# Kernel optimization log

Measured on AMD Instinct MI355X. Metric: run time of the kernel, lower is better.

The kernel has to match this reference:

```python
import jax, jax.numpy as jnp
import numpy as np

N_CHANNELS = 512
D_K = 64
N_HEADS = N_CHANNELS // D_K  # 8
SCALE = 1.0 / np.sqrt(np.sqrt(D_K))
EPS = 1e-8


def pixnorm(x, axis=-1):
    return x * jax.lax.rsqrt(jnp.mean(x * x, axis=axis, keepdims=True) + EPS)


def setup_inputs() -> dict:
    key = jax.random.key(0)
    k1, k2, k3 = jax.random.split(key, 3)
    x = jax.random.normal(k1, (16, N_CHANNELS, 32, 32), dtype=jnp.float32)
    # 1x1 conv weights (bias=False) stored as [out, in]
    w_proj = jax.random.normal(k2, (3 * N_CHANNELS, N_CHANNELS), dtype=jnp.float32) * (1.0 / np.sqrt(N_CHANNELS))
    w_out = jax.random.normal(k3, (N_CHANNELS, N_CHANNELS), dtype=jnp.float32) * (1.0 / np.sqrt(N_CHANNELS))
    return {"x": x, "w_proj": w_proj, "w_out": w_out}


def reference(x, w_proj, w_out):
    B, C, H, W = x.shape
    S = H * W
    # tokens: [B, S, C]
    xt = x.reshape(B, C, S).transpose(0, 2, 1)
    # 1x1 conv projection -> [B, S, 3C]
    h = jnp.einsum('bsc,oc->bso', xt, w_proj)
    qkv = h.reshape(B, S, N_HEADS, 3 * D_K)
    q, k, v = jnp.split(qkv, 3, axis=-1)  # each [B, S, H, d]
    q = pixnorm(q)
    k = pixnorm(k)
    v = pixnorm(v)
    attn = jnp.einsum('bihd,bjhd->bijh', q * SCALE, k * SCALE)
    attn = jax.nn.softmax(attn, axis=2)
    res = jnp.einsum('bijh,bjhd->bihd', attn, v)  # [B, S, H, d]
    res = res.reshape(B, S, C)
    res = jnp.einsum('bsc,oc->bso', res, w_out)
    res = res.transpose(0, 2, 1).reshape(B, C, H, W)
    return x + res
```

## Files before the change

kernel.cpp:

```cpp
#include <hip/hip_runtime.h>
#include <hip/hip_bf16.h>
#include <math.h>

typedef float f32x4 __attribute__((ext_vector_type(4)));
typedef __bf16 bf16x8 __attribute__((ext_vector_type(8)));
typedef __bf16 bf16x4 __attribute__((ext_vector_type(4)));
typedef unsigned u32x4 __attribute__((ext_vector_type(4)));

#define DEVFN static __device__ __forceinline__

DEVFN void gload16(const void* g, void* l) {
  __builtin_amdgcn_global_load_lds(
      (const __attribute__((address_space(1))) unsigned int*)g,
      (__attribute__((address_space(3))) unsigned int*)l, 16, 0, 0);
}

DEVFN f32x4 mfma16(bf16x8 a, bf16x8 b, f32x4 c) {
  return __builtin_amdgcn_mfma_f32_16x16x32_bf16(a, b, c, 0, 0, 0);
}

DEVFN unsigned cvtpk(float lo, float hi) {
  unsigned r;
  asm("v_cvt_pk_bf16_f32 %0, %1, %2" : "=v"(r) : "v"(lo), "v"(hi));
  return r;
}

#define WAITV4() asm volatile("s_waitcnt vmcnt(4)" ::: "memory")
#define WAITV0() asm volatile("s_waitcnt vmcnt(0)" ::: "memory")

__global__ __launch_bounds__(256) void transpose_x_k(
    const float* __restrict__ x, __bf16* __restrict__ xt,
    const float* __restrict__ wp, const float* __restrict__ wo,
    __bf16* __restrict__ wpb, __bf16* __restrict__ wob) {
  __shared__ float tile[64][65];
  int b = blockIdx.z, c0 = blockIdx.y * 64, s0 = blockIdx.x * 64;
  int t = threadIdx.x;
  int r = t >> 2, q = (t & 3) << 4;
  const float* src = x + ((size_t)(b * 512 + c0 + r)) * 1024 + s0 + q;
#pragma unroll
  for (int i = 0; i < 4; i++) {
    float4 f = *reinterpret_cast<const float4*>(src + i * 4);
    tile[r][q + i * 4 + 0] = f.x;
    tile[r][q + i * 4 + 1] = f.y;
    tile[r][q + i * 4 + 2] = f.z;
    tile[r][q + i * 4 + 3] = f.w;
  }
  int lid = (blockIdx.z * 8 + blockIdx.y) * 16 + blockIdx.x;
  int wi = lid * 512 + t * 2;
  if (wi < 786432) {
    float2 f = *reinterpret_cast<const float2*>(wp + wi);
    wpb[wi] = (__bf16)f.x;
    wpb[wi + 1] = (__bf16)f.y;
  } else {
    int j = wi - 786432;
    float2 f = *reinterpret_cast<const float2*>(wo + j);
    wob[j] = (__bf16)f.x;
    wob[j + 1] = (__bf16)f.y;
  }
  __syncthreads();
  bf16x8 o0, o1;
#pragma unroll
  for (int i = 0; i < 8; i++) o0[i] = (__bf16)tile[q + i][r];
#pragma unroll
  for (int i = 0; i < 8; i++) o1[i] = (__bf16)tile[q + 8 + i][r];
  __bf16* dst = xt + ((size_t)(b * 1024 + s0 + r)) * 512 + c0 + q;
  *reinterpret_cast<bf16x8*>(dst) = o0;
  *reinterpret_cast<bf16x8*>(dst + 8) = o1;
}

template <int MODE>
__global__ __launch_bounds__(256, 4) void gemm_bt_k(
    const __bf16* __restrict__ A, const __bf16* __restrict__ Bt,
    float* __restrict__ Cf, const float* __restrict__ Xres,
    __bf16* __restrict__ Qo, __bf16* __restrict__ Ko, __bf16* __restrict__ Vto) {
  __shared__ __attribute__((aligned(16))) char smem[49152];
  int p = blockIdx.x, xcd = p & 7, idx = p >> 3;
  int m0, n0, z;
  if (MODE == 2) {
    m0 = (xcd * 16 + idx / 12) * 128;
    n0 = (idx % 12) * 128;
    z = 0;
  } else {
    z = xcd * 2 + idx / 32;
    int rem = idx % 32;
    m0 = (rem >> 3) * 128;
    n0 = (rem & 7) * 128;
    Bt += (size_t)z * (1024L * 512);
  }
  int tid = threadIdx.x, wave = tid >> 6, lane = tid & 63;
  int fr = lane & 15, fq = lane >> 4;
  int wm = (wave >> 1) * 64, wn = (wave & 1) * 64;
  f32x4 acc[4][4] = {};
  int offs[2], rr[2], scc[2];
#pragma unroll
  for (int i = 0; i < 2; i++) {
    offs[i] = wave * 2048 + i * 1024 + lane * 16;
    rr[i] = offs[i] >> 6;
    scc[i] = (offs[i] & 63) ^ (((rr[i] ^ (rr[i] >> 2)) & 3) << 4);
  }
  int rdsw = (fr ^ (fr >> 2)) & 3;
  const char* Ap = (const char*)A;
  const char* Bp = (const char*)Bt;

#define GSTAGE(k0_, slot_)                                                      \
  {                                                                             \
    char* as_ = smem + (slot_)*16384;                                           \
    char* bs_ = as_ + 8192;                                                     \
    _Pragma("unroll") for (int i = 0; i < 2; i++)                               \
        gload16(Ap + (size_t)(m0 + rr[i]) * 1024 + (k0_)*2 + scc[i],            \
                as_ + offs[i]);                                                 \
    _Pragma("unroll") for (int i = 0; i < 2; i++)                               \
        gload16(Bp + (size_t)(n0 + rr[i]) * 1024 + (k0_)*2 + scc[i],            \
                bs_ + offs[i]);                                                 \
  }

  GSTAGE(0, 0);
  GSTAGE(32, 1);
#pragma unroll
  for (int t = 0; t < 16; t++) {
    if (t < 15) WAITV4(); else WAITV0();
    __builtin_amdgcn_s_barrier();
    __builtin_amdgcn_sched_barrier(0);
    const char* as = smem + (t % 3) * 16384;
    const char* bs = as + 8192;
    bf16x8 af[4], bfr[4];
#pragma unroll
    for (int mi = 0; mi < 4; mi++)
      af[mi] = *reinterpret_cast<const bf16x8*>(
          as + (wm + mi * 16 + fr) * 64 + ((fq ^ rdsw) << 4));
#pragma unroll
    for (int ni = 0; ni < 4; ni++)
      bfr[ni] = *reinterpret_cast<const bf16x8*>(
          bs + (wn + ni * 16 + fr) * 64 + ((fq ^ rdsw) << 4));
    if (t + 2 < 16) GSTAGE((t + 2) * 32, (t + 2) % 3);
    __builtin_amdgcn_s_setprio(1);
#pragma unroll
    for (int mi = 0; mi < 4; mi++)
#pragma unroll
      for (int ni = 0; ni < 4; ni++)
        acc[mi][ni] = mfma16(af[mi], bfr[ni], acc[mi][ni]);
    __builtin_amdgcn_s_setprio(0);
  }
#undef GSTAGE

  if (MODE == 1) {
    float* Co = Cf + (size_t)z * (512L * 1024);
    const float* Xr = Xres + (size_t)z * (512L * 1024);
#pragma unroll
    for (int mi = 0; mi < 4; mi++)
#pragma unroll
      for (int i = 0; i < 4; i++) {
        int row = m0 + wm + mi * 16 + fq * 4 + i;
#pragma unroll
        for (int ni = 0; ni < 4; ni++) {
          size_t idxo = (size_t)row * 1024 + n0 + wn + ni * 16 + fr;
          Co[idxo] = acc[mi][ni][i] + Xr[idxo];
        }
      }
  } else {
    int g0 = n0 + wn;
    int head = g0 / 192;
    int grp = (g0 >> 6) % 3;
    int b = m0 >> 10, sb = m0 & 1023;
    int bh = b * 8 + head;
    float nrm[4][4];
#pragma unroll
    for (int mi = 0; mi < 4; mi++)
#pragma unroll
      for (int i = 0; i < 4; i++) {
        float ss = 0.f;
#pragma unroll
        for (int ni = 0; ni < 4; ni++) ss += acc[mi][ni][i] * acc[mi][ni][i];
#pragma unroll
        for (int off = 1; off < 16; off <<= 1) ss += __shfl_xor(ss, off);
        float nv = rsqrtf(ss * (1.0f / 64.0f) + 1e-8f);
        if (grp == 0) nv *= 0.18033688011112042f;
        nrm[mi][i] = nv;
      }
    if (grp < 2) {
      __bf16* dst = (grp == 0 ? Qo : Ko) + (size_t)bh * 65536;
#pragma unroll
      for (int mi = 0; mi < 4; mi++)
#pragma unroll
        for (int i = 0; i < 4; i++) {
          int s = sb + wm + mi * 16 + fq * 4 + i;
#pragma unroll
          for (int ni = 0; ni < 4; ni++)
            dst[(size_t)s * 64 + ni * 16 + fr] = (__bf16)(acc[mi][ni][i] * nrm[mi][i]);
        }
    }
    __syncthreads();
    if (grp == 2) {
#pragma unroll
      for (int mi = 0; mi < 4; mi++)
#pragma unroll
        for (int i = 0; i < 4; i++) {
          int r = wm + mi * 16 + fq * 4 + i;
#pragma unroll
          for (int ni = 0; ni < 4; ni++) {
            int col2 = (2 * (ni * 16 + fr)) ^ ((r & 31) << 2);
            *(__bf16*)(smem + r * 128 + col2) = (__bf16)(acc[mi][ni][i] * nrm[mi][i]);
          }
        }
    }
    __syncthreads();
    if (grp == 2) {
      int sl = wm + lane;
      int l = sl & 63;
      int pl = ((l >> 2) & 3) * 16 + (l >> 4) * 4 + (l & 3);
      __bf16* vdst = Vto + (size_t)bh * 65536 + sb + (sl & 64) + pl;
#pragma unroll 8
      for (int d = 0; d < 64; d++) {
        __bf16 v = *(const __bf16*)(smem + sl * 128 + ((2 * d) ^ ((sl & 31) << 2)));
        vdst[(size_t)d * 1024] = v;
      }
    }
  }
}

__global__ __launch_bounds__(256, 4) void attn_k(const __bf16* __restrict__ Q,
                                                 const __bf16* __restrict__ Kb,
                                                 const __bf16* __restrict__ Vt,
                                                 __bf16* __restrict__ Res) {
  __shared__ __attribute__((aligned(16))) char lds[32768];
  int p = blockIdx.x;
  int v = (p & 7) * 128 + (p >> 3);
  int qt = v & 7, bh = v >> 3;
  int wave = threadIdx.x >> 6, lane = threadIdx.x & 63;
  int fr = lane & 15, fq = lane >> 4;
  const __bf16* Qb = Q + (size_t)bh * 65536;
  const char* Kbase = (const char*)(Kb + (size_t)bh * 65536);
  const char* Vbase = (const char*)(Vt + (size_t)bh * 65536);
  bf16x8 qf[2][2];
#pragma unroll
  for (int qs = 0; qs < 2; qs++)
#pragma unroll
    for (int kk = 0; kk < 2; kk++)
      qf[qs][kk] = *reinterpret_cast<const bf16x8*>(
          Qb + (size_t)(qt * 128 + qs * 64 + wave * 16 + fr) * 64 + kk * 32 + fq * 8);

  bf16x8 ones;
#pragma unroll
  for (int j = 0; j < 8; j++) ones[j] = (__bf16)1.0f;

  f32x4 oa[2][4] = {};
  f32x4 lacc[2] = {};

  int o0 = wave * 2048 + lane * 16;
  int o1 = o0 + 1024;
  int r0 = o0 >> 7, c0 = o0 & 127, r1 = o1 >> 7, c1 = o1 & 127;
  int s0 = c0 ^ ((r0 & 7) << 4), s1 = c1 ^ ((r1 & 7) << 4);
  int swr = (fr & 7) << 4;

#define STAGE(kt_, buf_)                                                        \
  {                                                                             \
    char* ks_ = lds + (buf_)*8192;                                              \
    char* vs_ = lds + 16384 + (buf_)*8192;                                      \
    gload16(Kbase + (size_t)(kt_)*8192 + r0 * 128 + s0, ks_ + o0);              \
    gload16(Kbase + (size_t)(kt_)*8192 + r1 * 128 + s1, ks_ + o1);              \
    gload16(Vbase + (size_t)r0 * 2048 + (kt_)*128 + s0, vs_ + o0);              \
    gload16(Vbase + (size_t)r1 * 2048 + (kt_)*128 + s1, vs_ + o1);              \
  }

#define QKT(buf_)                                                               \
  {                                                                             \
    const char* ksc_ = lds + (buf_)*8192;                                       \
    __builtin_amdgcn_s_setprio(1);                                              \
    _Pragma("unroll") for (int ni = 0; ni < 4; ni++) {                          \
      bf16x8 kf0 = *reinterpret_cast<const bf16x8*>(                            \
          ksc_ + (ni * 16 + fr) * 128 + ((fq * 16) ^ swr));                     \
      bf16x8 kf1 = *reinterpret_cast<const bf16x8*>(                            \
          ksc_ + (ni * 16 + fr) * 128 + ((64 + fq * 16) ^ swr));                \
      _Pragma("unroll") for (int qs = 0; qs < 2; qs++) {                        \
        sa[qs][ni] = mfma16(kf0, qf[qs][0], sa[qs][ni]);                        \
        sa[qs][ni] = mfma16(kf1, qf[qs][1], sa[qs][ni]);                        \
      }                                                                         \
    }                                                                           \
    __builtin_amdgcn_s_setprio(0);                                              \
  }

  STAGE(0, 0);
  STAGE(1, 1);
  WAITV4();
  __builtin_amdgcn_s_barrier();
  __builtin_amdgcn_sched_barrier(0);
  f32x4 sa[2][4] = {};
  QKT(0);
  for (int kt = 0; kt < 16; kt++) {
    int cur = kt & 1;
    const char* vsc = lds + 16384 + cur * 8192;
    bf16x8 pb[2][2];
#pragma unroll
    for (int qs = 0; qs < 2; qs++) {
#pragma unroll
      for (int ni = 0; ni < 4; ni++)
#pragma unroll
        for (int i = 0; i < 4; i++)
          sa[qs][ni][i] = __builtin_amdgcn_exp2f(sa[qs][ni][i]);
#pragma unroll
      for (int kk2 = 0; kk2 < 2; kk2++) {
        u32x4 u;
        u[0] = cvtpk(sa[qs][2 * kk2][0], sa[qs][2 * kk2][1]);
        u[1] = cvtpk(sa[qs][2 * kk2][2], sa[qs][2 * kk2][3]);
        u[2] = cvtpk(sa[qs][2 * kk2 + 1][0], sa[qs][2 * kk2 + 1][1]);
        u[3] = cvtpk(sa[qs][2 * kk2 + 1][2], sa[qs][2 * kk2 + 1][3]);
        pb[qs][kk2] = __builtin_bit_cast(bf16x8, u);
      }
      lacc[qs] = mfma16(ones, pb[qs][0], lacc[qs]);
      lacc[qs] = mfma16(ones, pb[qs][1], lacc[qs]);
    }
    __builtin_amdgcn_s_setprio(1);
#pragma unroll
    for (int nd = 0; nd < 4; nd++) {
      int vrow = (nd * 16 + fr) * 128;
#pragma unroll
      for (int kk2 = 0; kk2 < 2; kk2++) {
        bf16x8 vf = *reinterpret_cast<const bf16x8*>(
            vsc + vrow + ((fq * 32 + kk2 * 16) ^ swr));
#pragma unroll
        for (int qs = 0; qs < 2; qs++)
          oa[qs][nd] = mfma16(vf, pb[qs][kk2], oa[qs][nd]);
      }
    }
    __builtin_amdgcn_s_setprio(0);
    if (kt == 15) break;
    __builtin_amdgcn_s_barrier();
    if (kt + 2 < 16) {
      STAGE(kt + 2, cur);
      WAITV4();
    } else {
      WAITV0();
    }
    __builtin_amdgcn_s_barrier();
    __builtin_amdgcn_sched_barrier(0);
#pragma unroll
    for (int qs = 0; qs < 2; qs++)
#pragma unroll
      for (int ni = 0; ni < 4; ni++) sa[qs][ni] = (f32x4){0.f, 0.f, 0.f, 0.f};
    QKT(cur ^ 1);
  }
  int b = bh >> 3, hd = bh & 7;
#pragma unroll
  for (int qs = 0; qs < 2; qs++) {
    int q = qt * 128 + qs * 64 + wave * 16 + fr;
    float inv_l = 1.0f / lacc[qs][0];
    __bf16* dst = Res + ((size_t)(b * 1024 + q)) * 512 + hd * 64 + fq * 4;
#pragma unroll
    for (int nd = 0; nd < 4; nd++) {
      bf16x4 ov;
#pragma unroll
      for (int i = 0; i < 4; i++) ov[i] = (__bf16)(oa[qs][nd][i] * inv_l);
      *reinterpret_cast<bf16x4*>(dst + nd * 16) = ov;
    }
  }
#undef STAGE
#undef QKT
}

extern "C" void kernel_launch(void* const* d_in, const int* in_sizes, int n_in,
                              void* d_out, int out_size, void* d_ws, size_t ws_size,
                              hipStream_t stream) {
  const float* x = (const float*)d_in[0];
  const float* wp = (const float*)d_in[1];
  const float* wo = (const float*)d_in[2];
  float* out = (float*)d_out;
  char* w = (char*)d_ws;
  __bf16* wpb = (__bf16*)(w);
  __bf16* wob = (__bf16*)(w + 1572864);
  __bf16* xt = (__bf16*)(w + 2097152);
  __bf16* Qb = (__bf16*)(w + 18874368);
  __bf16* Kb = (__bf16*)(w + 35651584);
  __bf16* Vtb = (__bf16*)(w + 52428800);
  __bf16* resb = (__bf16*)(w + 69206016);

  transpose_x_k<<<dim3(16, 8, 16), 256, 0, stream>>>(x, xt, wp, wo, wpb, wob);
  gemm_bt_k<2><<<1536, 256, 0, stream>>>(xt, wpb, nullptr, nullptr, Qb, Kb, Vtb);
  attn_k<<<1024, 256, 0, stream>>>(Qb, Kb, Vtb, resb);
  gemm_bt_k<1><<<512, 256, 0, stream>>>(wob, resb, out, x, nullptr, nullptr,
                                        nullptr);
}
```

Before: 116.9 us.

## Double attention query tile per block and switch to triple-buffered K/V staging

Each attention block now processes 256 queries instead of 128 (four 64-row sub-tiles per wave), halving the grid to 512 blocks and halving total K/V tile loads from global memory. The K/V pipeline becomes a 3-slot ring in 48KB LDS with one barrier per iteration, and QK^T is computed in the same iteration instead of being software-pipelined one step ahead. The cost is more registers (launch bounds lowered to 2 blocks/CU), fewer blocks for load balance across CUs, and less overlap between the QK^T and PV phases.

Result: no change. 115.2 us (-1.5%).

```diff
diff --git a/kernel.cpp b/kernel.cpp
--- a/kernel.cpp
+++ b/kernel.cpp
@@ -218,33 +218,33 @@
   }
 }
 
-__global__ __launch_bounds__(256, 4) void attn_k(const __bf16* __restrict__ Q,
+__global__ __launch_bounds__(256, 2) void attn_k(const __bf16* __restrict__ Q,
                                                  const __bf16* __restrict__ Kb,
                                                  const __bf16* __restrict__ Vt,
                                                  __bf16* __restrict__ Res) {
-  __shared__ __attribute__((aligned(16))) char lds[32768];
+  __shared__ __attribute__((aligned(16))) char lds[49152];
   int p = blockIdx.x;
-  int v = (p & 7) * 128 + (p >> 3);
-  int qt = v & 7, bh = v >> 3;
+  int v = (p & 7) * 64 + (p >> 3);
+  int qt = v & 3, bh = v >> 2;
   int wave = threadIdx.x >> 6, lane = threadIdx.x & 63;
   int fr = lane & 15, fq = lane >> 4;
   const __bf16* Qb = Q + (size_t)bh * 65536;
   const char* Kbase = (const char*)(Kb + (size_t)bh * 65536);
   const char* Vbase = (const char*)(Vt + (size_t)bh * 65536);
-  bf16x8 qf[2][2];
-#pragma unroll
-  for (int qs = 0; qs < 2; qs++)
+  bf16x8 qf[4][2];
+#pragma unroll
+  for (int qs = 0; qs < 4; qs++)
 #pragma unroll
     for (int kk = 0; kk < 2; kk++)
       qf[qs][kk] = *reinterpret_cast<const bf16x8*>(
-          Qb + (size_t)(qt * 128 + qs * 64 + wave * 16 + fr) * 64 + kk * 32 + fq * 8);
+          Qb + (size_t)(qt * 256 + qs * 64 + wave * 16 + fr) * 64 + kk * 32 + fq * 8);
 
   bf16x8 ones;
 #pragma unroll
   for (int j = 0; j < 8; j++) ones[j] = (__bf16)1.0f;
 
-  f32x4 oa[2][4] = {};
-  f32x4 lacc[2] = {};
+  f32x4 oa[4][4] = {};
+  f32x4 lacc[4] = {};
 
   int o0 = wave * 2048 + lane * 16;
   int o1 = o0 + 1024;
@@ -252,46 +252,43 @@
   int s0 = c0 ^ ((r0 & 7) << 4), s1 = c1 ^ ((r1 & 7) << 4);
   int swr = (fr & 7) << 4;
 
-#define STAGE(kt_, buf_)                                                        \
+#define STAGE(kt_, slot_)                                                       \
   {                                                                             \
-    char* ks_ = lds + (buf_)*8192;                                              \
-    char* vs_ = lds + 16384 + (buf_)*8192;                                      \
+    char* ks_ = lds + (slot_)*16384;                                            \
+    char* vs_ = ks_ + 8192;                                                     \
     gload16(Kbase + (size_t)(kt_)*8192 + r0 * 128 + s0, ks_ + o0);              \
     gload16(Kbase + (size_t)(kt_)*8192 + r1 * 128 + s1, ks_ + o1);              \
     gload16(Vbase + (size_t)r0 * 2048 + (kt_)*128 + s0, vs_ + o0);              \
     gload16(Vbase + (size_t)r1 * 2048 + (kt_)*128 + s1, vs_ + o1);              \
   }
 
-#define QKT(buf_)                                                               \
-  {                                                                             \
-    const char* ksc_ = lds + (buf_)*8192;                                       \
-    __builtin_amdgcn_s_setprio(1);                                              \
-    _Pragma("unroll") for (int ni = 0; ni < 4; ni++) {                          \
-      bf16x8 kf0 = *reinterpret_cast<const bf16x8*>(                            \
-          ksc_ + (ni * 16 + fr) * 128 + ((fq * 16) ^ swr));                     \
-      bf16x8 kf1 = *reinterpret_cast<const bf16x8*>(                            \
-          ksc_ + (ni * 16 + fr) * 128 + ((64 + fq * 16) ^ swr));                \
-      _Pragma("unroll") for (int qs = 0; qs < 2; qs++) {                        \
-        sa[qs][ni] = mfma16(kf0, qf[qs][0], sa[qs][ni]);                        \
-        sa[qs][ni] = mfma16(kf1, qf[qs][1], sa[qs][ni]);                        \
-      }                                                                         \
-    }                                                                           \
-    __builtin_amdgcn_s_setprio(0);                                              \
-  }
-
   STAGE(0, 0);
   STAGE(1, 1);
-  WAITV4();
-  __builtin_amdgcn_s_barrier();
-  __builtin_amdgcn_sched_barrier(0);
-  f32x4 sa[2][4] = {};
-  QKT(0);
   for (int kt = 0; kt < 16; kt++) {
-    int cur = kt & 1;
-    const char* vsc = lds + 16384 + cur * 8192;
-    bf16x8 pb[2][2];
-#pragma unroll
-    for (int qs = 0; qs < 2; qs++) {
+    if (kt < 15) WAITV4(); else WAITV0();
+    __builtin_amdgcn_s_barrier();
+    __builtin_amdgcn_sched_barrier(0);
+    if (kt + 2 < 16) STAGE(kt + 2, (kt + 2) % 3);
+    const char* ksc = lds + (kt % 3) * 16384;
+    const char* vsc = ksc + 8192;
+    f32x4 sa[4][4] = {};
+    __builtin_amdgcn_s_setprio(1);
+#pragma unroll
+    for (int ni = 0; ni < 4; ni++) {
+      bf16x8 kf0 = *reinterpret_cast<const bf16x8*>(
+          ksc + (ni * 16 + fr) * 128 + ((fq * 16) ^ swr));
+      bf16x8 kf1 = *reinterpret_cast<const bf16x8*>(
+          ksc + (ni * 16 + fr) * 128 + ((64 + fq * 16) ^ swr));
+#pragma unroll
+      for (int qs = 0; qs < 4; qs++) {
+        sa[qs][ni] = mfma16(kf0, qf[qs][0], sa[qs][ni]);
+        sa[qs][ni] = mfma16(kf1, qf[qs][1], sa[qs][ni]);
+      }
+    }
+    __builtin_amdgcn_s_setprio(0);
+    bf16x8 pb[4][2];
+#pragma unroll
+    for (int qs = 0; qs < 4; qs++) {
 #pragma unroll
       for (int ni = 0; ni < 4; ni++)
 #pragma unroll
@@ -318,31 +315,16 @@
         bf16x8 vf = *reinterpret_cast<const bf16x8*>(
             vsc + vrow + ((fq * 32 + kk2 * 16) ^ swr));
 #pragma unroll
-        for (int qs = 0; qs < 2; qs++)
+        for (int qs = 0; qs < 4; qs++)
           oa[qs][nd] = mfma16(vf, pb[qs][kk2], oa[qs][nd]);
       }
     }
     __builtin_amdgcn_s_setprio(0);
-    if (kt == 15) break;
-    __builtin_amdgcn_s_barrier();
-    if (kt + 2 < 16) {
-      STAGE(kt + 2, cur);
-      WAITV4();
-    } else {
-      WAITV0();
-    }
-    __builtin_amdgcn_s_barrier();
-    __builtin_amdgcn_sched_barrier(0);
-#pragma unroll
-    for (int qs = 0; qs < 2; qs++)
-#pragma unroll
-      for (int ni = 0; ni < 4; ni++) sa[qs][ni] = (f32x4){0.f, 0.f, 0.f, 0.f};
-    QKT(cur ^ 1);
   }
   int b = bh >> 3, hd = bh & 7;
 #pragma unroll
-  for (int qs = 0; qs < 2; qs++) {
-    int q = qt * 128 + qs * 64 + wave * 16 + fr;
+  for (int qs = 0; qs < 4; qs++) {
+    int q = qt * 256 + qs * 64 + wave * 16 + fr;
     float inv_l = 1.0f / lacc[qs][0];
     __bf16* dst = Res + ((size_t)(b * 1024 + q)) * 512 + hd * 64 + fq * 4;
 #pragma unroll
@@ -354,7 +336,6 @@
     }
   }
 #undef STAGE
-#undef QKT
 }
 
 extern "C" void kernel_launch(void* const* d_in, const int* in_sizes, int n_in,
@@ -375,7 +356,7 @@
 
   transpose_x_k<<<dim3(16, 8, 16), 256, 0, stream>>>(x, xt, wp, wo, wpb, wob);
   gemm_bt_k<2><<<1536, 256, 0, stream>>>(xt, wpb, nullptr, nullptr, Qb, Kb, Vtb);
-  attn_k<<<1024, 256, 0, stream>>>(Qb, Kb, Vtb, resb);
+  attn_k<<<512, 256, 0, stream>>>(Qb, Kb, Vtb, resb);
   gemm_bt_k<1><<<512, 256, 0, stream>>>(wob, resb, out, x, nullptr, nullptr,
                                         nullptr);
 }
```
